# Kernel tuning notes

Measured on AMD Instinct MI355X. Metric: run time of the kernel, lower is better.

## Reference

```python
import jax, jax.numpy as jnp
import numpy as np

B, S, H, NH, EHH, L = 8, 4, 50, 200, 400, 2
HID = 128
FDIM = 44 + 20 + 15          # 79: atom one-hot + amino-acid one-hot + position one-hot
EDIM = 2 * FDIM + 3          # h_i, h_j, distance, bond, t -> 161


def setup_inputs() -> dict:
    key = jax.random.key(0)
    ks = jax.random.split(key, 32)
    inp = {}
    inp["t"] = jax.random.uniform(ks[0], (B,), dtype=jnp.float32)
    inp["x_h"] = jax.random.normal(ks[1], (B, S, H, 3), dtype=jnp.float32)
    inp["x_heavy"] = jax.random.normal(ks[2], (B, 1, NH, 3), dtype=jnp.float32)
    inp["bond_matrix_h_heavy"] = (jax.random.uniform(ks[3], (B, H, NH)) < 0.02).astype(jnp.float32)
    inp["edge_mask_h_heavy"] = jnp.ones((B, H, NH), jnp.float32)
    inp["edge_mask_h_h"] = jnp.ones((B, EHH), jnp.float32)
    inp["atom_mask"] = jnp.ones((B, H, 1), jnp.float32)
    sc = 0.02
    shapes = {"W1": (L, EDIM, HID), "b1": (L, HID), "W2": (L, HID, HID), "b2": (L, HID),
              "Wc1": (L, HID, HID), "bc1": (L, HID), "Wc2": (L, HID, 1),
              "Wn1": (L, FDIM + HID, HID), "bn1": (L, HID), "Wn2": (L, HID, FDIM), "bn2": (L, FDIM)}
    for i, (n, s) in enumerate(shapes.items()):
        inp[n] = jax.random.normal(ks[4 + i], s, dtype=jnp.float32) * sc
    inp["peptide_seq"] = jax.random.randint(ks[20], (B, 15), 0, 20)
    inp["atom_labels_heavy"] = jax.random.randint(ks[21], (B, NH), 0, 44)
    inp["atom_labels_h"] = jax.random.randint(ks[22], (B, H), 0, 44)
    inp["amino_acid_pos_heavy"] = jax.random.randint(ks[23], (B, NH), 1, 16)
    inp["amino_acid_pos_h"] = jax.random.randint(ks[24], (B, H), 1, 16)
    inp["edges_h_h"] = jax.random.randint(ks[25], (B, EHH, 2), 0, H)
    inp["bound_atom"] = jax.random.randint(ks[26], (B, H), 0, NH)
    return inp


def _embed(labels, pos, peptide_seq):
    # one_hot(atom,44) ++ one_hot(seq[pos-1],20) ++ one_hot(pos-1,15)
    aa = jnp.take_along_axis(peptide_seq, pos - 1, axis=1)
    return jnp.concatenate([jax.nn.one_hot(labels, 44, dtype=jnp.float32),
                            jax.nn.one_hot(aa, 20, dtype=jnp.float32),
                            jax.nn.one_hot(pos - 1, 15, dtype=jnp.float32)], axis=-1)


def _gather_nodes(feat, idx):
    # feat [B,S,N,D], idx [B,E] -> [B,S,E,D]
    return jnp.take_along_axis(feat, idx[:, None, :, None], axis=2)


def _seg(data, ids, n):
    # data [B,S,E,D], ids [B,E] -> scatter-add over edges -> [B,S,n,D]
    f = jax.vmap(lambda d, i: jax.ops.segment_sum(jnp.swapaxes(d, 0, 1), i, num_segments=n))
    return jnp.swapaxes(f(data, ids), 1, 2)


def _forward(t, x_h, x_heavy, bond_hm, em_hheavy, em_hh, atom_mask,
             W1, b1, W2, b2, Wc1, bc1, Wc2, Wn1, bn1, Wn2, bn2,
             peptide_seq, atom_labels_heavy, atom_labels_h, pos_heavy, pos_h,
             edges_h_h, bound_atom):
    Bq, Sq, Hq, _ = x_h.shape
    Nh = x_heavy.shape[2]
    xhv = jnp.broadcast_to(x_heavy, (Bq, Sq, Nh, 3))
    emb_h = _embed(atom_labels_h, pos_h, peptide_seq)          # [B,H,79]
    emb_hv = _embed(atom_labels_heavy, pos_heavy, peptide_seq)  # [B,NH,79]
    # absolute coords: x_h relative to its bound heavy atom
    x_h_abs = x_h + jnp.take_along_axis(xhv, bound_atom[:, None, :, None], axis=2)
    x = jnp.concatenate([x_h_abs, xhv], axis=2)                 # [B,S,N,3]
    feat = jnp.concatenate([emb_h, emb_hv], axis=1)             # [B,N,79]
    feat = jnp.broadcast_to(feat[:, None], (Bq, Sq) + feat.shape[1:])
    bond = jnp.concatenate([jnp.zeros((Bq, Hq, Hq), bond_hm.dtype), bond_hm], axis=-1)  # [B,H,N]
    # edge indices: sparse h-h edges, then full h x heavy grid (row-major, cols offset by H)
    grid_r = jnp.repeat(jnp.arange(Hq), Nh)
    grid_c = Hq + jnp.tile(jnp.arange(Nh), Hq)
    edge_row = jnp.concatenate([edges_h_h[..., 0], jnp.broadcast_to(grid_r, (Bq, Hq * Nh))], axis=-1)
    edge_col = jnp.concatenate([edges_h_h[..., 1], jnp.broadcast_to(grid_c, (Bq, Hq * Nh))], axis=-1)
    emask = jnp.concatenate([em_hh, em_hheavy.reshape(Bq, -1)], axis=-1)[:, None, :, None]  # [B,1,E,1]
    bond_e = jax.vmap(lambda bm, r, c: bm[r, c])(bond, edge_row, edge_col)[:, None, :, None]
    x0 = x
    for l in range(W1.shape[0]):
        xi = _gather_nodes(x, edge_row)
        xj = _gather_nodes(x, edge_col)
        diff = xi - xj                                          # [B,S,E,3]
        dist = jnp.linalg.norm(diff, axis=-1, keepdims=True)    # [B,S,E,1]
        hi = _gather_nodes(feat, edge_row)
        hj = _gather_nodes(feat, edge_col)
        t_e = jnp.broadcast_to(t[:, None, None, None], dist.shape)
        ef = jnp.concatenate([hi, hj, dist, jnp.broadcast_to(bond_e, dist.shape), t_e], axis=-1)
        m = jax.nn.silu(ef @ W1[l] + b1[l])
        m = jax.nn.silu(m @ W2[l] + b2[l]) * emask              # masked messages [B,S,E,HID]
        cw = jax.nn.silu(m @ Wc1[l] + bc1[l]) @ Wc2[l]          # [B,S,E,1]
        agg_x = _seg(diff * cw, edge_row, Hq)                   # [B,S,H,3]
        agg_m = _seg(m, edge_row, Hq)                           # [B,S,H,HID]
        h_h = feat[:, :, :Hq]
        h_out = h_h + jax.nn.silu(jnp.concatenate([h_h, agg_m], axis=-1) @ Wn1[l] + bn1[l]) @ Wn2[l] + bn2[l]
        x = jnp.concatenate([x[:, :, :Hq] + agg_x, x[:, :, Hq:]], axis=2)
        feat = jnp.concatenate([h_out, feat[:, :, Hq:]], axis=2)
    pred = (x[:, :, :Hq] - x0[:, :, :Hq]) * atom_mask[:, None, :, :]
    return pred


def reference(t, x_h, x_heavy, bond_matrix_h_heavy, edge_mask_h_heavy, edge_mask_h_h, atom_mask,
              W1, b1, W2, b2, Wc1, bc1, Wc2, Wn1, bn1, Wn2, bn2,
              peptide_seq, atom_labels_heavy, atom_labels_h, amino_acid_pos_heavy, amino_acid_pos_h,
              edges_h_h, bound_atom):
    return _forward(t, x_h, x_heavy, bond_matrix_h_heavy, edge_mask_h_heavy, edge_mask_h_h, atom_mask,
                    W1, b1, W2, b2, Wc1, bc1, Wc2, Wn1, bn1, Wn2, bn2,
                    peptide_seq, atom_labels_heavy, atom_labels_h, amino_acid_pos_heavy, amino_acid_pos_h,
                    edges_h_h, bound_atom)
```

## Files before the change

### kernel.cpp

```cpp
#include <hip/hip_runtime.h>
#include <math.h>

#define B_     8
#define S_     4
#define H_     50
#define NH_    200
#define EHH_   400
#define L_     2
#define HID_   128
#define FDIM_  79
#define EDIM_  161
#define NN_    250
#define NROW_  1600
#define BS_    32
#define FS_    80
#define MSTR_  136
#define NDIM_  207
#define HVB_   1600

#define OFF_FEATH  0
#define OFF_X0     128000
#define OFF_X1     160000
#define OFF_X0H    192000
#define OFF_HHCOL  198400
#define OFF_HHEM   201600
#define OFF_HHOFF  204800
#define OFF_HIW1   205312
#define OFF_HJW1   614912
#define OFF_WP     1434112

typedef __attribute__((ext_vector_type(8))) short short8;
typedef __attribute__((ext_vector_type(4))) float f32x4;

__device__ __forceinline__ float silu_(float v) {
    return v * __builtin_amdgcn_rcpf(1.0f + __expf(-v));
}
__device__ __forceinline__ unsigned short f2bf(float f) {
    unsigned int u = __float_as_uint(f);
    unsigned int r = (u + 0x7fffu + ((u >> 16) & 1u)) >> 16;
    return (unsigned short)r;
}

#define HV_BLKS_    1600
#define PACK_BLKS_  256
#define SORT_BLKS_  8
#define HROW_BLKS_  200
#define FEAT_BLKS_  125
#define XI_BLKS_    32
#define SETUP_BLKS_ (HV_BLKS_ + PACK_BLKS_ + SORT_BLKS_ + HROW_BLKS_ + FEAT_BLKS_ + XI_BLKS_)

__global__ __launch_bounds__(256) void k_setup(
    const float* __restrict__ x_h, const float* __restrict__ x_hv,
    const int* __restrict__ bound,
    const int* __restrict__ ehh, const float* __restrict__ em_hh,
    const float* __restrict__ W1, const float* __restrict__ b1,
    const float* __restrict__ t_in,
    const float* __restrict__ W2, const float* __restrict__ Wc1,
    const int* __restrict__ lab_h, const int* __restrict__ pos_h,
    const int* __restrict__ lab_hv, const int* __restrict__ pos_hv,
    const int* __restrict__ pep,
    float* __restrict__ feat_h,
    float* __restrict__ x0, float* __restrict__ x1, float* __restrict__ x0h,
    int* __restrict__ hhcol, float* __restrict__ hhem, int* __restrict__ hhoff,
    float* __restrict__ hiW1, float* __restrict__ hjW1,
    unsigned short* __restrict__ Wp)
{
    int blk = blockIdx.x, t = threadIdx.x;
    if (blk < HV_BLKS_) {
        int g = blk*256 + t;
        int l = g / 204800;
        int r = g - l*204800;
        int node = r >> 7, col = r & 127;
        int b = node / NH_;
        int label = lab_hv[node], pos = pos_hv[node];
        int aa = pep[b*15 + pos - 1];
        const float* W1l = W1 + l*EDIM_*HID_;
        float hj = W1l[(FDIM_ + label)*HID_ + col]
                 + W1l[(FDIM_ + 44 + aa)*HID_ + col]
                 + W1l[(FDIM_ + 64 + pos - 1)*HID_ + col];
        hjW1[(size_t)(HVB_ + l*1600 + node)*HID_ + col] = hj;
        return;
    }
    blk -= HV_BLKS_;
    if (blk < PACK_BLKS_) {
        int g = blk*256 + t;
        int idx = g & 16383;
        int lm  = g >> 14;
        int l = lm >> 1, mat = lm & 1;
        int j   = idx & 7;
        int l15 = (idx >> 3) & 15;
        int qq  = (idx >> 7) & 3;
        int nt  = (idx >> 9) & 7;
        int kc  = (idx >> 12) & 3;
        int n = nt*16 + l15;
        int k = kc*32 + qq*8 + j;
        const float* W = (mat == 0 ? W2 : Wc1) + l*HID_*HID_;
        Wp[g] = f2bf(W[k*HID_ + n]);
        return;
    }
    blk -= PACK_BLKS_;
    if (blk < SORT_BLKS_) {
        int b = blk;
        __shared__ int scnt[64];
        __shared__ int srow[EHH_], scol[EHH_];
        __shared__ float sem[EHH_];
        if (t < 64) scnt[t] = 0;
        __syncthreads();
        for (int e = t; e < EHH_; e += 256) {
            int r = ehh[(b*EHH_ + e)*2 + 0];
            srow[e] = r;
            scol[e] = ehh[(b*EHH_ + e)*2 + 1];
            sem[e]  = em_hh[b*EHH_ + e];
            atomicAdd(&scnt[r], 1);
        }
        __syncthreads();
        if (t == 0) {
            int acc = 0;
            for (int i = 0; i < H_; ++i) { int v = scnt[i]; scnt[i] = acc; acc += v; }
        }
        __syncthreads();
        if (t < 51) hhoff[b*64 + t] = (t < H_) ? scnt[t] : EHH_;
        __syncthreads();
        for (int e = t; e < EHH_; e += 256) {
            int r = srow[e];
            int pos = atomicAdd(&scnt[r], 1);
            hhcol[b*EHH_ + pos] = scol[e];
            hhem [b*EHH_ + pos] = sem[e];
        }
        return;
    }
    blk -= SORT_BLKS_;
    if (blk < HROW_BLKS_) {
        int g = blk*256 + t;
        int node = g >> 7, col = g & 127;
        int b = node / H_;
        int label = lab_h[node], pos = pos_h[node];
        int aa = pep[b*15 + pos - 1];
        const float* W1l = W1;
        float hi = W1l[label*HID_ + col]
                 + W1l[(44 + aa)*HID_ + col]
                 + W1l[(64 + pos - 1)*HID_ + col]
                 + b1[col]
                 + t_in[b] * W1l[160*HID_ + col];
        float hj = W1l[(FDIM_ + label)*HID_ + col]
                 + W1l[(FDIM_ + 44 + aa)*HID_ + col]
                 + W1l[(FDIM_ + 64 + pos - 1)*HID_ + col];
        int h = node % H_;
        #pragma unroll
        for (int s = 0; s < S_; ++s) {
            int row = (b*S_ + s)*H_ + h;
            hiW1[(size_t)row*HID_ + col] = hi;
            hjW1[(size_t)row*HID_ + col] = hj;
        }
        return;
    }
    blk -= HROW_BLKS_;
    if (blk < FEAT_BLKS_) {
        int g = blk*256 + t;
        int node = g / FS_, f = g % FS_;
        int b = node / H_, h = node % H_;
        int label = lab_h[node], pos = pos_h[node];
        int aa = pep[b*15 + pos - 1];
        float v = 0.f;
        if (f < 44)      v = (f == label)          ? 1.0f : 0.0f;
        else if (f < 64) v = ((f - 44) == aa)      ? 1.0f : 0.0f;
        else if (f < 79) v = ((f - 64) == pos - 1) ? 1.0f : 0.0f;
        #pragma unroll
        for (int s = 0; s < S_; ++s)
            feat_h[((b*S_ + s)*H_ + h)*FS_ + f] = v;
        return;
    }
    blk -= FEAT_BLKS_;
    {
        int g = blk*256 + t;
        if (g >= BS_*NN_) return;
        int bs = g / NN_, n = g % NN_;
        int b = bs / S_;
        if (n < H_) {
            int ba = bound[b*H_ + n];
            for (int d = 0; d < 3; ++d) {
                float v = x_h[(bs*H_ + n)*3 + d] + x_hv[(b*NH_ + ba)*3 + d];
                x0[g*4 + d] = v;
                x0h[(bs*H_ + n)*4 + d] = v;
            }
        } else {
            int nh = n - H_;
            for (int d = 0; d < 3; ++d) {
                float v = x_hv[(b*NH_ + nh)*3 + d];
                x0[g*4 + d] = v;
                x1[g*4 + d] = v;
            }
        }
    }
}

__global__ __launch_bounds__(512) void k_edge_mlp(
    const float* __restrict__ xin, const float* __restrict__ hiW1g,
    const float* __restrict__ hjW1,
    const int* __restrict__ hhcol, const float* __restrict__ hhem,
    const int* __restrict__ hhoff,
    const float* __restrict__ em_hv, const float* __restrict__ bond_in,
    const float* __restrict__ W1,
    const float* __restrict__ b2, const float* __restrict__ bc1,
    const float* __restrict__ Wc2,
    const unsigned short* __restrict__ Wp, int l,
    const float* __restrict__ Wn1, const float* __restrict__ bn1,
    const float* __restrict__ Wn2, const float* __restrict__ bn2,
    const float* __restrict__ b1, const float* __restrict__ t_in,
    float* __restrict__ feat_h, float* __restrict__ xout,
    float* __restrict__ hiW1w, float* __restrict__ hjW1w,
    const float* __restrict__ x0h, const float* __restrict__ amask,
    float* __restrict__ out, int do_w1)
{
    __shared__ unsigned short s_wp[2*16384];
    __shared__ unsigned short s_m[8][16][MSTR_];
    __shared__ float s_hi[2][HID_];
    __shared__ float s_cc[5][HID_];
    __shared__ float s_mr[2][4][HID_];
    __shared__ float s_xr[2][4][4];

    const int t = threadIdx.x, lane = t & 63, w = t >> 6;
    const int l15 = lane & 15, q = lane >> 4;
    const int r  = w >> 2;
    const int wr = w & 3;
    const int node0 = blockIdx.x*2;
    const int node  = node0 + r;
    const int bs = node / H_, h = node - bs*H_;
    const int b  = bs / S_;
    const int hb = (l ? 4800 : 0) + bs*H_;

    {
        const float4* src = (const float4*)(Wp + (size_t)l*32768);
        float4* dst = (float4*)s_wp;
        #pragma unroll
        for (int i = 0; i < 8; ++i) dst[t + i*512] = src[t + i*512];
    }
    const float* W1l = W1 + l*EDIM_*HID_;
    if (t < 128) {
        s_hi[0][t] = hiW1g[(size_t)(l*1600 + node0)*HID_ + t];
    } else if (t < 256) {
        int c = t - 128;
        s_hi[1][c] = hiW1g[(size_t)(l*1600 + node0 + 1)*HID_ + c];
    } else if (t < 384) {
        int c = t - 256;
        s_cc[0][c] = W1l[158*HID_ + c];
        s_cc[3][c] = bc1[l*HID_ + c];
    } else {
        int c = t - 384;
        s_cc[1][c] = W1l[159*HID_ + c];
        s_cc[2][c] = b2 [l*HID_ + c];
        s_cc[4][c] = Wc2[l*HID_ + c];
    }

    const int hh0 = hhoff[b*64 + h];
    const int cnt = hhoff[b*64 + h + 1] - hh0;
    const int E   = cnt + NH_;
    const int NT  = (E + 15) >> 4;

    const float xi0 = xin[(bs*NN_ + h)*4 + 0];
    const float xi1 = xin[(bs*NN_ + h)*4 + 1];
    const float xi2 = xin[(bs*NN_ + h)*4 + 2];

    auto gather = [&](int e, float& d0, float& d1, float& d2,
                      float& dist, float& bnd, float& em, int& jj) {
        if (e < E) {
            int col;
            if (e < cnt) {
                col = hhcol[b*EHH_ + hh0 + e];
                em  = hhem [b*EHH_ + hh0 + e];
                jj  = hb + col;
            } else {
                int cc = e - cnt;
                col = H_ + cc;
                em  = em_hv [(b*H_ + h)*NH_ + cc];
                bnd = bond_in[(b*H_ + h)*NH_ + cc];
                jj  = HVB_ + l*1600 + b*NH_ + cc;
            }
            d0 = xi0 - xin[(bs*NN_ + col)*4 + 0];
            d1 = xi1 - xin[(bs*NN_ + col)*4 + 1];
            d2 = xi2 - xin[(bs*NN_ + col)*4 + 2];
            dist = sqrtf(d0*d0 + d1*d1 + d2*d2);
        }
    };

    float macc[8] = {0.f,0.f,0.f,0.f,0.f,0.f,0.f,0.f};
    float xacc = 0.f;
    __syncthreads();

    float cd0=0.f, cd1=0.f, cd2=0.f, cdist=0.f, cbnd=0.f, cem=0.f;
    int   cjj = hb;
    if (lane < 16) gather(wr*16 + lane, cd0, cd1, cd2, cdist, cbnd, cem, cjj);
    float distb = __shfl(cdist, l15, 64);
    float bndb  = __shfl(cbnd,  l15, 64);
    int   jjb   = __shfl(cjj,   l15, 64);
    float4 pr[8];
    {
        const float* pj = hjW1 + (size_t)jjb*HID_ + q*8;
        #pragma unroll
        for (int kc = 0; kc < 4; ++kc) {
            pr[2*kc]   = *(const float4*)(pj + kc*32);
            pr[2*kc+1] = *(const float4*)(pj + kc*32 + 4);
        }
    }

    for (int ti = wr; ti < NT; ti += 4) {
        const int nx = ti + 4;
        const bool hasNext = (nx < NT);

        float nd0=0.f, nd1=0.f, nd2=0.f, ndist=0.f, nbnd=0.f, nem=0.f;
        int   njj = hb;
        if (hasNext && lane < 16)
            gather(nx*16 + lane, nd0, nd1, nd2, ndist, nbnd, nem, njj);

        short8 afrag[4];
        #pragma unroll
        for (int kc = 0; kc < 4; ++kc) {
            int k0 = kc*32 + q*8;
            float4 c0 = pr[2*kc];
            float4 c1 = pr[2*kc+1];
            float4 h0 = *(const float4*)&s_hi[r][k0];
            float4 h1 = *(const float4*)&s_hi[r][k0 + 4];
            float4 wa0= *(const float4*)&s_cc[0][k0];
            float4 wa1= *(const float4*)&s_cc[0][k0 + 4];
            float4 wb0= *(const float4*)&s_cc[1][k0];
            float4 wb1= *(const float4*)&s_cc[1][k0 + 4];
            short8 fr;
            fr[0] = (short)f2bf(silu_(h0.x + c0.x + distb*wa0.x + bndb*wb0.x));
            fr[1] = (short)f2bf(silu_(h0.y + c0.y + distb*wa0.y + bndb*wb0.y));
            fr[2] = (short)f2bf(silu_(h0.z + c0.z + distb*wa0.z + bndb*wb0.z));
            fr[3] = (short)f2bf(silu_(h0.w + c0.w + distb*wa0.w + bndb*wb0.w));
            fr[4] = (short)f2bf(silu_(h1.x + c1.x + distb*wa1.x + bndb*wb1.x));
            fr[5] = (short)f2bf(silu_(h1.y + c1.y + distb*wa1.y + bndb*wb1.y));
            fr[6] = (short)f2bf(silu_(h1.z + c1.z + distb*wa1.z + bndb*wb1.z));
            fr[7] = (short)f2bf(silu_(h1.w + c1.w + distb*wa1.w + bndb*wb1.w));
            afrag[kc] = fr;
        }

        float ndistb = 0.f, nbndb = 0.f;
        if (hasNext) {
            ndistb = __shfl(ndist, l15, 64);
            nbndb  = __shfl(nbnd,  l15, 64);
            int njjb = __shfl(njj, l15, 64);
            const float* pj = hjW1 + (size_t)njjb*HID_ + q*8;
            #pragma unroll
            for (int kc = 0; kc < 4; ++kc) {
                pr[2*kc]   = *(const float4*)(pj + kc*32);
                pr[2*kc+1] = *(const float4*)(pj + kc*32 + 4);
            }
        }

        float em4[4];
        #pragma unroll
        for (int rr = 0; rr < 4; ++rr) em4[rr] = __shfl(cem, q*4 + rr, 64);
        #pragma unroll
        for (int nt = 0; nt < 8; ++nt) {
            float bias = s_cc[2][nt*16 + l15];
            f32x4 c = {bias, bias, bias, bias};
            #pragma unroll
            for (int kc = 0; kc < 4; ++kc) {
                short8 bf = *(const short8*)&s_wp[((kc*8 + nt)*64 + lane)*8];
                c = __builtin_amdgcn_mfma_f32_16x16x32_bf16(afrag[kc], bf, c, 0, 0, 0);
            }
            #pragma unroll
            for (int rr = 0; rr < 4; ++rr) {
                float mv = silu_(c[rr]) * em4[rr];
                s_m[w][q*4 + rr][nt*16 + l15] = f2bf(mv);
                macc[nt] += mv;
            }
        }
        __builtin_amdgcn_wave_barrier();

        short8 af2[4];
        #pragma unroll
        for (int kc = 0; kc < 4; ++kc)
            af2[kc] = *(const short8*)&s_m[w][l15][kc*32 + q*8];
        float p[4] = {0.f, 0.f, 0.f, 0.f};
        #pragma unroll
        for (int nt = 0; nt < 8; ++nt) {
            float bias = s_cc[3][nt*16 + l15];
            f32x4 c = {bias, bias, bias, bias};
            #pragma unroll
            for (int kc = 0; kc < 4; ++kc) {
                short8 bf = *(const short8*)&s_wp[16384 + ((kc*8 + nt)*64 + lane)*8];
                c = __builtin_amdgcn_mfma_f32_16x16x32_bf16(af2[kc], bf, c, 0, 0, 0);
            }
            float wcv = s_cc[4][nt*16 + l15];
            #pragma unroll
            for (int rr = 0; rr < 4; ++rr)
                p[rr] += silu_(c[rr]) * wcv;
        }
        #pragma unroll
        for (int m = 1; m < 16; m <<= 1) {
            #pragma unroll
            for (int rr = 0; rr < 4; ++rr) p[rr] += __shfl_xor(p[rr], m, 64);
        }
        #pragma unroll
        for (int rr = 0; rr < 4; ++rr) {
            float sd0 = __shfl(cd0, q*4 + rr, 64);
            float sd1 = __shfl(cd1, q*4 + rr, 64);
            float sd2 = __shfl(cd2, q*4 + rr, 64);
            if (l15 < 3) {
                float dsel = (l15 == 0) ? sd0 : ((l15 == 1) ? sd1 : sd2);
                xacc += dsel * p[rr];
            }
        }
        __builtin_amdgcn_wave_barrier();

        cd0 = nd0; cd1 = nd1; cd2 = nd2; cem = nem;
        distb = ndistb; bndb = nbndb;
    }

    #pragma unroll
    for (int nt = 0; nt < 8; ++nt) {
        macc[nt] += __shfl_xor(macc[nt], 16, 64);
        macc[nt] += __shfl_xor(macc[nt], 32, 64);
    }
    if (q == 0) {
        #pragma unroll
        for (int nt = 0; nt < 8; ++nt) s_mr[r][wr][nt*16 + l15] = macc[nt];
    }
    xacc += __shfl_xor(xacc, 16, 64);
    xacc += __shfl_xor(xacc, 32, 64);
    if (q == 0 && l15 < 3) s_xr[r][wr][l15] = xacc;
    __syncthreads();

    float* su = (float*)s_wp;
    if (t < 416) {
        int g = t / 208, k = t - g*208;
        float v = 0.f;
        if (k < FDIM_)      v = feat_h[(node0 + g)*FS_ + k];
        else if (k < NDIM_) {
            int c = k - FDIM_;
            v = s_mr[g][0][c] + s_mr[g][1][c] + s_mr[g][2][c] + s_mr[g][3][c];
        }
        su[g*208 + k] = v;
    }
    __syncthreads();
    {
        const float* Wn1l = Wn1 + l*NDIM_*HID_;
        int kh = t >> 8, g = (t >> 7) & 1, c = t & 127;
        float acc = 0.f;
        if (kh == 0) {
            const float* wp = Wn1l + c;
            const float* sp = su + g*208;
            #pragma unroll 8
            for (int k = 0; k < 104; ++k)
                acc += sp[k] * wp[(size_t)k*HID_];
        } else {
            const float* wp = Wn1l + (size_t)104*HID_ + c;
            const float* sp = su + g*208 + 104;
            #pragma unroll 8
            for (int k = 0; k < 103; ++k)
                acc += sp[k] * wp[(size_t)k*HID_];
        }
        su[1024 + t] = acc;
    }
    __syncthreads();
    if (t < 256) {
        int c = t & 127;
        su[512 + t] = silu_(su[1024 + t] + su[1280 + t] + bn1[l*HID_ + c]);
    }
    __syncthreads();
    if (t < 316) {
        const float* Wn2l = Wn2 + l*HID_*FDIM_;
        int kh = t / 158, r2 = t - kh*158;
        int g = r2 / FDIM_, c = r2 - g*FDIM_;
        const float* wp = Wn2l + (size_t)(kh*64)*FDIM_ + c;
        const float* up = su + 512 + g*HID_ + kh*64;
        float acc = 0.f;
        #pragma unroll 8
        for (int k = 0; k < 64; ++k)
            acc += up[k] * wp[(size_t)k*FDIM_];
        su[1536 + t] = acc;
    }
    __syncthreads();
    if (t < 158) {
        int g = t / FDIM_, c = t - g*FDIM_;
        float nf = su[g*208 + c] + su[1536 + t] + su[1694 + t] + bn2[l*FDIM_ + c];
        feat_h[(node0 + g)*FS_ + c] = nf;
        su[g*208 + c] = nf;
    } else if (t >= 256 && t < 262) {
        int ix = t - 256, g = ix / 3, d = ix - g*3;
        int ng = node0 + g;
        int bsg = ng / H_, hg = ng - bsg*H_;
        float xv = xin[(bsg*NN_ + hg)*4 + d]
                 + s_xr[g][0][d] + s_xr[g][1][d] + s_xr[g][2][d] + s_xr[g][3][d];
        if (do_w1) {
            xout[(bsg*NN_ + hg)*4 + d] = xv;
        } else {
            int bg = bsg / S_;
            out[ng*3 + d] = (xv - x0h[ng*4 + d]) * amask[bg*H_ + hg];
        }
    }
    if (!do_w1) return;
    __syncthreads();
    {
        const float* W1n = W1 + EDIM_*HID_;
        int sel = t >> 8, g = (t >> 7) & 1, c = t & 127;
        const float* wp = W1n + (size_t)(sel ? FDIM_ : 0)*HID_ + c;
        const float* sp = su + g*208;
        float acc = 0.f;
        #pragma unroll 8
        for (int f = 0; f < FDIM_; ++f)
            acc += sp[f] * wp[(size_t)f*HID_];
        int ng = node0 + g;
        if (sel == 0) {
            int bg = (ng / H_) / S_;
            hiW1w[(size_t)(1600 + ng)*HID_ + c] =
                acc + b1[HID_ + c] + t_in[bg]*W1n[160*HID_ + c];
        } else {
            hjW1w[(size_t)(4800 + ng)*HID_ + c] = acc;
        }
    }
}

extern "C" void kernel_launch(void* const* d_in, const int* in_sizes, int n_in,
                              void* d_out, int out_size, void* d_ws, size_t ws_size,
                              hipStream_t stream)
{
    const float* t_in  = (const float*)d_in[0];
    const float* x_h   = (const float*)d_in[1];
    const float* x_hv  = (const float*)d_in[2];
    const float* bond  = (const float*)d_in[3];
    const float* em_hv = (const float*)d_in[4];
    const float* em_hh = (const float*)d_in[5];
    const float* amask = (const float*)d_in[6];
    const float* W1    = (const float*)d_in[7];
    const float* b1    = (const float*)d_in[8];
    const float* W2    = (const float*)d_in[9];
    const float* b2    = (const float*)d_in[10];
    const float* Wc1   = (const float*)d_in[11];
    const float* bc1   = (const float*)d_in[12];
    const float* Wc2   = (const float*)d_in[13];
    const float* Wn1   = (const float*)d_in[14];
    const float* bn1   = (const float*)d_in[15];
    const float* Wn2   = (const float*)d_in[16];
    const float* bn2   = (const float*)d_in[17];
    const int* pep     = (const int*)d_in[18];
    const int* lab_hv  = (const int*)d_in[19];
    const int* lab_h   = (const int*)d_in[20];
    const int* pos_hv  = (const int*)d_in[21];
    const int* pos_h   = (const int*)d_in[22];
    const int* ehh     = (const int*)d_in[23];
    const int* bound   = (const int*)d_in[24];

    float* ws     = (float*)d_ws;
    float* feat_h = ws + OFF_FEATH;
    float* x0     = ws + OFF_X0;
    float* x1     = ws + OFF_X1;
    float* x0h    = ws + OFF_X0H;
    int*   hhcol  = (int*)(ws + OFF_HHCOL);
    float* hhem   = ws + OFF_HHEM;
    int*   hhoff  = (int*)(ws + OFF_HHOFF);
    float* hiW1   = ws + OFF_HIW1;
    float* hjW1   = ws + OFF_HJW1;
    unsigned short* Wp = (unsigned short*)(ws + OFF_WP);

    hipLaunchKernelGGL(k_setup, dim3(SETUP_BLKS_), dim3(256), 0, stream,
                       x_h, x_hv, bound, ehh, em_hh,
                       W1, b1, t_in, W2, Wc1,
                       lab_h, pos_h, lab_hv, pos_hv, pep,
                       feat_h, x0, x1, x0h, hhcol, hhem, hhoff,
                       hiW1, hjW1, Wp);

    hipLaunchKernelGGL(k_edge_mlp, dim3(NROW_/2), dim3(512), 0, stream,
                       x0, hiW1, hjW1, hhcol, hhem, hhoff, em_hv, bond,
                       W1, b2, bc1, Wc2, Wp, 0,
                       Wn1, bn1, Wn2, bn2, b1, t_in,
                       feat_h, x1, hiW1, hjW1, x0h, amask,
                       (float*)d_out, 1);

    hipLaunchKernelGGL(k_edge_mlp, dim3(NROW_/2), dim3(512), 0, stream,
                       x1, hiW1, hjW1, hhcol, hhem, hhoff, em_hv, bond,
                       W1, b2, bc1, Wc2, Wp, 1,
                       Wn1, bn1, Wn2, bn2, b1, t_in,
                       feat_h, x1, hiW1, hjW1, x0h, amask,
                       (float*)d_out, 0);
}
```

Before: 373.4 us.

## Assign one node per wave and process eight nodes per block

Result: faster. 322.7 us (median of 3 runs) (-13.6%).

```diff
diff --git a/kernel.cpp b/kernel.cpp
--- a/kernel.cpp
+++ b/kernel.cpp
@@ -214,17 +214,15 @@
 {
     __shared__ unsigned short s_wp[2*16384];
     __shared__ unsigned short s_m[8][16][MSTR_];
-    __shared__ float s_hi[2][HID_];
+    __shared__ float s_hi[8][HID_];
     __shared__ float s_cc[5][HID_];
-    __shared__ float s_mr[2][4][HID_];
-    __shared__ float s_xr[2][4][4];
+    __shared__ float s_mr[8][HID_];
+    __shared__ float s_xr[8][4];
 
     const int t = threadIdx.x, lane = t & 63, w = t >> 6;
     const int l15 = lane & 15, q = lane >> 4;
-    const int r  = w >> 2;
-    const int wr = w & 3;
-    const int node0 = blockIdx.x*2;
-    const int node  = node0 + r;
+    const int node0 = blockIdx.x*8;
+    const int node  = node0 + w;
     const int bs = node / H_, h = node - bs*H_;
     const int b  = bs / S_;
     const int hb = (l ? 4800 : 0) + bs*H_;
@@ -236,20 +234,18 @@
         for (int i = 0; i < 8; ++i) dst[t + i*512] = src[t + i*512];
     }
     const float* W1l = W1 + l*EDIM_*HID_;
+    #pragma unroll
+    for (int i = 0; i < 2; ++i) {
+        int idx = i*512 + t;
+        int g = idx >> 7, c = idx & 127;
+        s_hi[g][c] = hiW1g[(size_t)(l*1600 + node0 + g)*HID_ + c];
+    }
     if (t < 128) {
-        s_hi[0][t] = hiW1g[(size_t)(l*1600 + node0)*HID_ + t];
-    } else if (t < 256) {
-        int c = t - 128;
-        s_hi[1][c] = hiW1g[(size_t)(l*1600 + node0 + 1)*HID_ + c];
-    } else if (t < 384) {
-        int c = t - 256;
-        s_cc[0][c] = W1l[158*HID_ + c];
-        s_cc[3][c] = bc1[l*HID_ + c];
-    } else {
-        int c = t - 384;
-        s_cc[1][c] = W1l[159*HID_ + c];
-        s_cc[2][c] = b2 [l*HID_ + c];
-        s_cc[4][c] = Wc2[l*HID_ + c];
+        s_cc[0][t] = W1l[158*HID_ + t];
+        s_cc[1][t] = W1l[159*HID_ + t];
+        s_cc[2][t] = b2 [l*HID_ + t];
+        s_cc[3][t] = bc1[l*HID_ + t];
+        s_cc[4][t] = Wc2[l*HID_ + t];
     }
 
     const int hh0 = hhoff[b*64 + h];
@@ -289,7 +285,7 @@
 
     float cd0=0.f, cd1=0.f, cd2=0.f, cdist=0.f, cbnd=0.f, cem=0.f;
     int   cjj = hb;
-    if (lane < 16) gather(wr*16 + lane, cd0, cd1, cd2, cdist, cbnd, cem, cjj);
+    if (lane < 16) gather(lane, cd0, cd1, cd2, cdist, cbnd, cem, cjj);
     float distb = __shfl(cdist, l15, 64);
     float bndb  = __shfl(cbnd,  l15, 64);
     int   jjb   = __shfl(cjj,   l15, 64);
@@ -303,8 +299,8 @@
         }
     }
 
-    for (int ti = wr; ti < NT; ti += 4) {
-        const int nx = ti + 4;
+    for (int ti = 0; ti < NT; ++ti) {
+        const int nx = ti + 1;
         const bool hasNext = (nx < NT);
 
         float nd0=0.f, nd1=0.f, nd2=0.f, ndist=0.f, nbnd=0.f, nem=0.f;
@@ -318,8 +314,8 @@
             int k0 = kc*32 + q*8;
             float4 c0 = pr[2*kc];
             float4 c1 = pr[2*kc+1];
-            float4 h0 = *(const float4*)&s_hi[r][k0];
-            float4 h1 = *(const float4*)&s_hi[r][k0 + 4];
+            float4 h0 = *(const float4*)&s_hi[w][k0];
+            float4 h1 = *(const float4*)&s_hi[w][k0 + 4];
             float4 wa0= *(const float4*)&s_cc[0][k0];
             float4 wa1= *(const float4*)&s_cc[0][k0 + 4];
             float4 wb0= *(const float4*)&s_cc[1][k0];
@@ -417,74 +413,62 @@
     }
     if (q == 0) {
         #pragma unroll
-        for (int nt = 0; nt < 8; ++nt) s_mr[r][wr][nt*16 + l15] = macc[nt];
+        for (int nt = 0; nt < 8; ++nt) s_mr[w][nt*16 + l15] = macc[nt];
     }
     xacc += __shfl_xor(xacc, 16, 64);
     xacc += __shfl_xor(xacc, 32, 64);
-    if (q == 0 && l15 < 3) s_xr[r][wr][l15] = xacc;
+    if (q == 0 && l15 < 3) s_xr[w][l15] = xacc;
     __syncthreads();
 
     float* su = (float*)s_wp;
-    if (t < 416) {
-        int g = t / 208, k = t - g*208;
-        float v = 0.f;
-        if (k < FDIM_)      v = feat_h[(node0 + g)*FS_ + k];
-        else if (k < NDIM_) {
-            int c = k - FDIM_;
-            v = s_mr[g][0][c] + s_mr[g][1][c] + s_mr[g][2][c] + s_mr[g][3][c];
-        }
+    for (int idx = t; idx < 8*208; idx += 512) {
+        int g = idx / 208, k = idx - g*208;
+        float v;
+        if (k < FDIM_) v = feat_h[(node0 + g)*FS_ + k];
+        else           v = s_mr[g][k - FDIM_];
         su[g*208 + k] = v;
     }
     __syncthreads();
     {
         const float* Wn1l = Wn1 + l*NDIM_*HID_;
-        int kh = t >> 8, g = (t >> 7) & 1, c = t & 127;
-        float acc = 0.f;
-        if (kh == 0) {
+        #pragma unroll
+        for (int pass = 0; pass < 2; ++pass) {
+            int task = pass*512 + t;
+            int g = task >> 7, c = task & 127;
+            const float* sp = su + g*208;
             const float* wp = Wn1l + c;
-            const float* sp = su + g*208;
+            float acc = 0.f;
             #pragma unroll 8
-            for (int k = 0; k < 104; ++k)
+            for (int k = 0; k < NDIM_; ++k)
                 acc += sp[k] * wp[(size_t)k*HID_];
-        } else {
-            const float* wp = Wn1l + (size_t)104*HID_ + c;
-            const float* sp = su + g*208 + 104;
-            #pragma unroll 8
-            for (int k = 0; k < 103; ++k)
-                acc += sp[k] * wp[(size_t)k*HID_];
-        }
-        su[1024 + t] = acc;
+            su[2048 + task] = silu_(acc + bn1[l*HID_ + c]);
+        }
     }
     __syncthreads();
-    if (t < 256) {
-        int c = t & 127;
-        su[512 + t] = silu_(su[1024 + t] + su[1280 + t] + bn1[l*HID_ + c]);
-    }
-    __syncthreads();
-    if (t < 316) {
+    {
         const float* Wn2l = Wn2 + l*HID_*FDIM_;
-        int kh = t / 158, r2 = t - kh*158;
-        int g = r2 / FDIM_, c = r2 - g*FDIM_;
-        const float* wp = Wn2l + (size_t)(kh*64)*FDIM_ + c;
-        const float* up = su + 512 + g*HID_ + kh*64;
-        float acc = 0.f;
-        #pragma unroll 8
-        for (int k = 0; k < 64; ++k)
-            acc += up[k] * wp[(size_t)k*FDIM_];
-        su[1536 + t] = acc;
-    }
-    __syncthreads();
-    if (t < 158) {
-        int g = t / FDIM_, c = t - g*FDIM_;
-        float nf = su[g*208 + c] + su[1536 + t] + su[1694 + t] + bn2[l*FDIM_ + c];
-        feat_h[(node0 + g)*FS_ + c] = nf;
-        su[g*208 + c] = nf;
-    } else if (t >= 256 && t < 262) {
-        int ix = t - 256, g = ix / 3, d = ix - g*3;
+        #pragma unroll
+        for (int pass = 0; pass < 2; ++pass) {
+            int task = pass*512 + t;
+            int g = task >> 7, c = task & 127;
+            if (c < FDIM_) {
+                const float* up = su + 2048 + g*HID_;
+                const float* wp = Wn2l + c;
+                float acc = bn2[l*FDIM_ + c];
+                #pragma unroll 8
+                for (int k = 0; k < HID_; ++k)
+                    acc += up[k] * wp[(size_t)k*FDIM_];
+                float nf = su[g*208 + c] + acc;
+                feat_h[(node0 + g)*FS_ + c] = nf;
+                su[g*208 + c] = nf;
+            }
+        }
+    }
+    if (t < 24) {
+        int g = t / 3, d = t - (t/3)*3;
         int ng = node0 + g;
         int bsg = ng / H_, hg = ng - bsg*H_;
-        float xv = xin[(bsg*NN_ + hg)*4 + d]
-                 + s_xr[g][0][d] + s_xr[g][1][d] + s_xr[g][2][d] + s_xr[g][3][d];
+        float xv = xin[(bsg*NN_ + hg)*4 + d] + s_xr[g][d];
         if (do_w1) {
             xout[(bsg*NN_ + hg)*4 + d] = xv;
         } else {
@@ -496,20 +480,24 @@
     __syncthreads();
     {
         const float* W1n = W1 + EDIM_*HID_;
-        int sel = t >> 8, g = (t >> 7) & 1, c = t & 127;
-        const float* wp = W1n + (size_t)(sel ? FDIM_ : 0)*HID_ + c;
-        const float* sp = su + g*208;
-        float acc = 0.f;
-        #pragma unroll 8
-        for (int f = 0; f < FDIM_; ++f)
-            acc += sp[f] * wp[(size_t)f*HID_];
-        int ng = node0 + g;
-        if (sel == 0) {
-            int bg = (ng / H_) / S_;
-            hiW1w[(size_t)(1600 + ng)*HID_ + c] =
-                acc + b1[HID_ + c] + t_in[bg]*W1n[160*HID_ + c];
-        } else {
-            hjW1w[(size_t)(4800 + ng)*HID_ + c] = acc;
+        #pragma unroll
+        for (int pass = 0; pass < 4; ++pass) {
+            int task = pass*512 + t;
+            int c = task & 127, g = (task >> 7) & 7, sel = task >> 10;
+            const float* sp = su + g*208;
+            const float* wp = W1n + (size_t)(sel ? FDIM_ : 0)*HID_ + c;
+            float acc = 0.f;
+            #pragma unroll 8
+            for (int f = 0; f < FDIM_; ++f)
+                acc += sp[f] * wp[(size_t)f*HID_];
+            int ng = node0 + g;
+            if (sel == 0) {
+                int bg = (ng / H_) / S_;
+                hiW1w[(size_t)(1600 + ng)*HID_ + c] =
+                    acc + b1[HID_ + c] + t_in[bg]*W1n[160*HID_ + c];
+            } else {
+                hjW1w[(size_t)(4800 + ng)*HID_ + c] = acc;
+            }
         }
     }
 }
@@ -563,14 +551,14 @@
                        feat_h, x0, x1, x0h, hhcol, hhem, hhoff,
                        hiW1, hjW1, Wp);
 
-    hipLaunchKernelGGL(k_edge_mlp, dim3(NROW_/2), dim3(512), 0, stream,
+    hipLaunchKernelGGL(k_edge_mlp, dim3(NROW_/8), dim3(512), 0, stream,
                        x0, hiW1, hjW1, hhcol, hhem, hhoff, em_hv, bond,
                        W1, b2, bc1, Wc2, Wp, 0,
                        Wn1, bn1, Wn2, bn2, b1, t_in,
                        feat_h, x1, hiW1, hjW1, x0h, amask,
                        (float*)d_out, 1);
 
-    hipLaunchKernelGGL(k_edge_mlp, dim3(NROW_/2), dim3(512), 0, stream,
+    hipLaunchKernelGGL(k_edge_mlp, dim3(NROW_/8), dim3(512), 0, stream,
                        x1, hiW1, hjW1, hhcol, hhem, hhoff, em_hv, bond,
                        W1, b2, bc1, Wc2, Wp, 1,
                        Wn1, bn1, Wn2, bn2, b1, t_in,
```
